# Performance work log

Hardware: AMD Instinct MI355X
Metric: run time of the kernel (lower is better)

Reference implementation:

```python
import jax, jax.numpy as jnp
import numpy as np
from jax import lax

NF = 64
KS = 3
PAD = 1
TOPK = 2
DG = 8          # deformable_groups
N = KS * KS     # 9 sampling points


def conv3x3(x, w, b):
    y = lax.conv_general_dilated(x, w, (1, 1), 'SAME',
                                 dimension_numbers=('NCHW', 'OIHW', 'NCHW'))
    return y + b[None, :, None, None]


def lrelu(x):
    return jnp.where(x >= 0, x, 0.1 * x)


def dsp_sample(x, feat, w_om, b_om):
    """Modulated deformable sampling (DSP_sep2): returns the N bilinearly
    sampled, mask-modulated taps per pixel, shape (B, C, N, H, W)."""
    B, C, H, W = x.shape
    Cg = C // DG
    om = conv3x3(feat, w_om, b_om)              # (B, 3*DG*N, H, W)
    o1, o2, m = jnp.split(om, 3, axis=1)
    off_y = o1.reshape(B, DG, N, H, W)
    off_x = o2.reshape(B, DG, N, H, W)
    mask = jax.nn.sigmoid(m).reshape(B, DG, 1, N, H * W)
    kk = (jnp.arange(KS) - PAD).astype(jnp.float32)
    kdy = jnp.repeat(kk, KS)                    # (N,) kernel row offsets
    kdx = jnp.tile(kk, KS)                      # (N,) kernel col offsets
    ii = jnp.arange(H, dtype=jnp.float32)
    jj = jnp.arange(W, dtype=jnp.float32)
    ys = ii[None, None, None, :, None] + kdy[None, None, :, None, None] + off_y
    xs = jj[None, None, None, None, :] + kdx[None, None, :, None, None] + off_x
    y0 = jnp.floor(ys)
    x0 = jnp.floor(xs)
    xf = x.reshape(B, DG, Cg, H * W)
    out = jnp.zeros((B, DG, Cg, N, H * W), x.dtype)
    # bilinear interpolation with zero padding outside the image
    for dy in (0.0, 1.0):
        for dx in (0.0, 1.0):
            yi = y0 + dy
            xi = x0 + dx
            wgt = (1.0 - jnp.abs(ys - yi)) * (1.0 - jnp.abs(xs - xi))
            valid = (yi >= 0) & (yi <= H - 1) & (xi >= 0) & (xi <= W - 1)
            lin = (jnp.clip(yi, 0, H - 1) * W + jnp.clip(xi, 0, W - 1)).astype(jnp.int32)
            g = jnp.take_along_axis(xf[:, :, :, None, :],
                                    lin.reshape(B, DG, 1, N, H * W), axis=-1)
            out = out + g * jnp.where(valid, wgt, 0.0).reshape(B, DG, 1, N, H * W)
    return (out * mask).reshape(B, C, N, H, W)


def setup_inputs() -> dict:
    key = jax.random.key(0)
    ks = jax.random.split(key, 9)
    B, C, H, W = 2, NF, 192, 192

    def rn(k, s, sc=1.0):
        return jax.random.normal(k, s, jnp.float32) * sc

    return {
        'query': rn(ks[0], (B, C, H, W)),
        'key':   rn(ks[1], (B, C, H, W)),
        'value': rn(ks[2], (B, C, H, W)),
        'w1': rn(ks[3], (C, 2 * C, 3, 3), 0.05), 'b1': rn(ks[4], (C,), 0.05),
        'w2': rn(ks[5], (C, C, 3, 3), 0.05),     'b2': rn(ks[6], (C,), 0.05),
        'w_om': rn(ks[7], (3 * DG * N, C, 3, 3), 0.01),
        'b_om': rn(ks[8], (3 * DG * N,), 0.01),
    }


def reference(query, key, value, w1, b1, w2, b2, w_om, b_om):
    B, C, H, W = query.shape
    HW = H * W
    feat = lrelu(conv3x3(jnp.concatenate([query, key], axis=1), w1, b1))
    feat = lrelu(conv3x3(feat, w2, b2))
    # deformable sampled keys: (B, C, N, H, W) -> (B, HW, N, C)
    key_off = dsp_sample(key, feat, w_om, b_om).transpose(0, 3, 4, 2, 1).reshape(B, HW, N, C)
    q = query.reshape(B, C, HW).transpose(0, 2, 1)            # (B, HW, C)
    rel = jnp.einsum('bpnc,bpc->bpn', key_off, q)             # relevance scores
    topv, topi = lax.top_k(rel, TOPK)                         # (B, HW, TOPK)
    corr = jax.nn.softmax(topv, axis=-1)
    val_off = dsp_sample(value, feat, w_om, b_om).transpose(0, 3, 4, 2, 1).reshape(B, HW, N, C)
    k_sel = jnp.take_along_axis(key_off, topi[..., None], axis=2)  # (B, HW, TOPK, C)
    v_sel = jnp.take_along_axis(val_off, topi[..., None], axis=2)
    k_upd = jnp.einsum('bptc,bpt->bpc', k_sel, corr)
    v_out = jnp.einsum('bptc,bpt->bpc', v_sel, corr).transpose(0, 2, 1)  # (B, C, HW)
    weight = jnp.einsum('bpc,bpc->bp', q, k_upd)              # (B, HW)
    return (weight, v_out)
```

## Files before the change

kernel.cpp:

```cpp
#include <hip/hip_runtime.h>
#include <math.h>

#define H_  192
#define W_  192
#define HW_ (192 * 192)
#define B_  2
#define C_  64
#define PW_ 194

typedef __attribute__((ext_vector_type(8))) short short8;
typedef __attribute__((ext_vector_type(4))) short short4v;
typedef __attribute__((ext_vector_type(4))) float float4v;
typedef _Float16 __attribute__((ext_vector_type(8))) half8;

union hbits { _Float16 f; short s; };
__device__ __forceinline__ void split2(float x, short& h, short& l) {
    _Float16 hf = (_Float16)x;
    float r = (x - (float)hf) * 4096.f;
    _Float16 lf = (_Float16)r;
    hbits u;
    u.f = hf; h = u.s;
    u.f = lf; l = u.s;
}

__device__ __forceinline__ float bilin_dot(const float* __restrict__ pl,
                                           float ys, float xs, int c4,
                                           float4v q4) {
    float y0 = floorf(ys), x0 = floorf(xs);
    float fy = ys - y0, fx = xs - x0;
    int iy = (int)y0, ix = (int)x0;
    float acc = 0.f;
    #pragma unroll
    for (int dy = 0; dy < 2; ++dy) {
        #pragma unroll
        for (int dx = 0; dx < 2; ++dx) {
            int yy = iy + dy, xx = ix + dx;
            float wgt = (dy ? fy : 1.f - fy) * (dx ? fx : 1.f - fx);
            bool valid = (yy >= 0) && (yy < H_) && (xx >= 0) && (xx < W_);
            int yc = min(max(yy, 0), H_ - 1);
            int xc = min(max(xx, 0), W_ - 1);
            const float4v v = *(const float4v*)(pl + (size_t)(yc * W_ + xc) * 64 + c4);
            float d = v[0] * q4[0] + v[1] * q4[1] + v[2] * q4[2] + v[3] * q4[3];
            acc += valid ? wgt * d : 0.f;
        }
    }
    return acc;
}
__device__ __forceinline__ float4v bilin_v4(const float* __restrict__ pl,
                                            float ys, float xs, int c4) {
    float y0 = floorf(ys), x0 = floorf(xs);
    float fy = ys - y0, fx = xs - x0;
    int iy = (int)y0, ix = (int)x0;
    float4v acc;
    acc[0] = acc[1] = acc[2] = acc[3] = 0.f;
    #pragma unroll
    for (int dy = 0; dy < 2; ++dy) {
        #pragma unroll
        for (int dx = 0; dx < 2; ++dx) {
            int yy = iy + dy, xx = ix + dx;
            float wgt = (dy ? fy : 1.f - fy) * (dx ? fx : 1.f - fx);
            bool valid = (yy >= 0) && (yy < H_) && (xx >= 0) && (xx < W_);
            float wz = valid ? wgt : 0.f;
            int yc = min(max(yy, 0), H_ - 1);
            int xc = min(max(xx, 0), W_ - 1);
            const float4v v = *(const float4v*)(pl + (size_t)(yc * W_ + xc) * 64 + c4);
            #pragma unroll
            for (int r = 0; r < 4; ++r) acc[r] += wz * v[r];
        }
    }
    return acc;
}

__global__ __launch_bounds__(256) void prep_w_k(
    const float* __restrict__ w1, const float* __restrict__ w2,
    const float* __restrict__ wom,
    short* __restrict__ pw1, short* __restrict__ pw2, short* __restrict__ pwom)
{
    int idx = blockIdx.x * 256 + threadIdx.x;
    int arr;
    if (idx < 144 * 512) { arr = 0; }
    else if (idx < (144 + 72) * 512) { arr = 1; idx -= 144 * 512; }
    else if (idx < (144 + 72 + 252) * 512) { arr = 2; idx -= (144 + 72) * 512; }
    else return;
    int frag = idx >> 9, within = idx & 511;
    int lane = within >> 3, j = within & 7;
    int KS   = (arr == 0) ? 4 : 2;
    int mt   = frag / (9 * KS);
    int rem  = frag % (9 * KS);
    int kk   = rem / KS;
    int s    = rem % KS;
    int co   = mt * 16 + (lane & 15);
    int c    = s * 32 + (lane >> 4) * 8 + j;
    float v = 0.f;
    if (arr == 0)      v = w1[(co * 128 + c) * 9 + kk];
    else if (arr == 1) v = w2[(co * 64 + c) * 9 + kk];
    else if (co < 216) v = wom[(co * 64 + c) * 9 + kk];
    short h, l;
    split2(v, h, l);
    short* dst = (arr == 0) ? pw1 : (arr == 1) ? pw2 : pwom;
    size_t base = (size_t)frag * 1024 + lane * 8 + j;
    dst[base]       = h;
    dst[base + 512] = l;
}

__global__ __launch_bounds__(256) void pack_qk(
    const float* __restrict__ q, const float* __restrict__ k,
    short* __restrict__ qk2)
{
    __shared__ float sm[128][65];
    const int tid = threadIdx.x;
    const int p0  = blockIdx.x * 64;
    const int b   = blockIdx.y;
    const int pp  = tid & 63;
    const int r0  = tid >> 6;
    #pragma unroll
    for (int c = r0; c < 128; c += 4) {
        const float* src = (c < 64) ? q : k;
        sm[c][pp] = src[(size_t)(b * 64 + (c & 63)) * HW_ + p0 + pp];
    }
    __syncthreads();
    for (int idx = tid; idx < 64 * 128; idx += 256) {
        int pxw = idx >> 7, ci = idx & 127;
        short h, l;
        split2(sm[ci][pxw], h, l);
        int p  = p0 + pxw;
        int rr = p / W_, cc = p - rr * W_;
        short* dstp = qk2 + ((size_t)(b * PW_ + rr + 1) * PW_ + cc + 1) * 256;
        dstp[ci]       = h;
        dstp[128 + ci] = l;
    }
}

__global__ __launch_bounds__(256) void zero_borders(
    short* __restrict__ f1p, short* __restrict__ f2p, short* __restrict__ qk2)
{
    const int prow = blockIdx.x;
    const int b    = blockIdx.y;
    const int z    = blockIdx.z;
    short* dst = (z == 0) ? f1p : (z == 1) ? f2p : qk2;
    const int nc = (z == 2) ? 256 : 128;
    dst += (size_t)(b * PW_ + prow) * PW_ * nc;
    if (prow == 0 || prow == PW_ - 1) {
        for (int idx = threadIdx.x; idx < PW_ * nc; idx += 256) dst[idx] = 0;
    } else {
        for (int idx = threadIdx.x; idx < nc; idx += 256) {
            dst[idx] = 0;
            dst[(size_t)(PW_ - 1) * nc + idx] = 0;
        }
    }
}

__global__ __launch_bounds__(256) void nchw_to_nhwc(
    const float* __restrict__ key, const float* __restrict__ value,
    float* __restrict__ kT, float* __restrict__ vT)
{
    __shared__ float sm[64][65];
    const int tid = threadIdx.x;
    const int p0  = blockIdx.x * 64;
    const int b   = blockIdx.y;
    const float* src = blockIdx.z ? value : key;
    float*       dst = blockIdx.z ? vT    : kT;
    const int pp = tid & 63;
    const int r0 = tid >> 6;
    #pragma unroll
    for (int c = r0; c < 64; c += 4)
        sm[c][pp] = src[(size_t)(b * 64 + c) * HW_ + p0 + pp];
    __syncthreads();
    const int cc = tid & 63;
    #pragma unroll
    for (int pw = r0; pw < 64; pw += 4)
        dst[((size_t)b * HW_ + p0 + pw) * 64 + cc] = sm[cc][pw];
}

template<int CIN, int MT, bool LRELU, int OUTMODE>
__global__ __launch_bounds__(256) void conv_direct(
    const short* __restrict__ in, const short* __restrict__ pw,
    const float* __restrict__ bias, void* __restrict__ outv)
{
    constexpr int KS  = CIN / 32;
    constexpr int MTW = MT / 2;

    const int tid  = threadIdx.x;
    const int lane = tid & 63;
    const int w    = tid >> 6;
    const int wh   = w & 1;
    const int wn   = w >> 1;
    const int quad = lane >> 4;
    const int nn   = lane & 15;

    const int flat = blockIdx.x;
    const int xcd  = flat & 7;
    const int cc_  = flat >> 3;
    const int b    = xcd >> 2;
    const int r4   = xcd & 3;
    const int i    = r4 * 48 + cc_ / 3;
    const int j0   = (cc_ % 3) * 64;
    const int mt0  = wh * MTW;

    constexpr float CSC = 1.f / 4096.f;

    float4v accM[MTW][2];
    #pragma unroll
    for (int m = 0; m < MTW; ++m)
        #pragma unroll
        for (int t = 0; t < 2; ++t)
            #pragma unroll
            for (int r = 0; r < 4; ++r) accM[m][t][r] = 0.f;

    float4v zvec;
    zvec[0] = zvec[1] = zvec[2] = zvec[3] = 0.f;

    for (int ky = 0; ky < 3; ++ky) {
        const short* rowp = in + ((size_t)(b * PW_ + (i + ky)) * PW_) * (2 * CIN);
        #pragma unroll
        for (int kx = 0; kx < 3; ++kx) {
            const int kk = ky * 3 + kx;
            #pragma unroll
            for (int s = 0; s < KS; ++s) {
                half8 bh[2], bl[2];
                #pragma unroll
                for (int t2 = 0; t2 < 2; ++t2) {
                    const int pcol = j0 + kx + (wn * 2 + t2) * 16 + nn;
                    const short* bp = rowp + (size_t)pcol * (2 * CIN)
                                    + s * 32 + quad * 8;
                    bh[t2] = *(const half8*)bp;
                    bl[t2] = *(const half8*)(bp + CIN);
                }
                #pragma unroll
                for (int m = 0; m < MTW; ++m) {
                    const short* ap = pw
                        + ((size_t)(((mt0 + m) * 9 + kk) * KS + s)) * 1024
                        + lane * 8;
                    half8 ah = *(const half8*)ap;
                    half8 al = *(const half8*)(ap + 512);
                    float4v t0, t1;
                    accM[m][0] = __builtin_amdgcn_mfma_f32_16x16x32_f16(ah, bh[0], accM[m][0], 0, 0, 0);
                    t0         = __builtin_amdgcn_mfma_f32_16x16x32_f16(ah, bl[0], zvec,       0, 0, 0);
                    accM[m][1] = __builtin_amdgcn_mfma_f32_16x16x32_f16(ah, bh[1], accM[m][1], 0, 0, 0);
                    t1         = __builtin_amdgcn_mfma_f32_16x16x32_f16(ah, bl[1], zvec,       0, 0, 0);
                    t0         = __builtin_amdgcn_mfma_f32_16x16x32_f16(al, bh[0], t0,         0, 0, 0);
                    t1         = __builtin_amdgcn_mfma_f32_16x16x32_f16(al, bh[1], t1,         0, 0, 0);
                    #pragma unroll
                    for (int r = 0; r < 4; ++r) {
                        accM[m][0][r] += t0[r] * CSC;
                        accM[m][1][r] += t1[r] * CSC;
                    }
                }
            }
        }
    }

    #pragma unroll
    for (int m = 0; m < MTW; ++m) {
        const int co0 = (mt0 + m) * 16 + quad * 4;
        #pragma unroll
        for (int t2 = 0; t2 < 2; ++t2) {
            const int t = wn * 2 + t2;
            if (OUTMODE == 0) {
                const size_t pp = ((size_t)(b * PW_ + i + 1) * PW_
                                   + (j0 + t * 16 + nn + 1)) * 128;
                short* feat = (short*)outv;
                short4v hv, lv;
                #pragma unroll
                for (int r = 0; r < 4; ++r) {
                    float x = accM[m][t2][r] + bias[co0 + r];
                    if (LRELU) x = (x >= 0.f) ? x : 0.1f * x;
                    short h, l;
                    split2(x, h, l);
                    hv[r] = h; lv[r] = l;
                }
                *(short4v*)(feat + pp + co0)      = hv;
                *(short4v*)(feat + pp + 64 + co0) = lv;
            } else {
                if (co0 < 216) {
                    const int p = i * W_ + j0 + t * 16 + nn;
                    float* om = (float*)outv;
                    float4v v;
                    #pragma unroll
                    for (int r = 0; r < 4; ++r)
                        v[r] = accM[m][t2][r] + bias[co0 + r];
                    *(float4v*)(om + ((size_t)b * HW_ + p) * 216 + co0) = v;
                }
            }
        }
    }
}

__global__ __launch_bounds__(256) void sampler_k(
    const float* __restrict__ query, const float* __restrict__ kT,
    const float* __restrict__ vT, const float* __restrict__ om,
    float* __restrict__ out_w, float* __restrict__ out_v)
{
    __shared__ float sq[16 * 68];
    const int tid  = threadIdx.x;
    const int bb   = blockIdx.x;
    const int b    = bb / 2304;
    const int pblk = (bb - b * 2304) * 16;

    #pragma unroll
    for (int k = 0; k < 4; ++k) {
        int idx = tid + k * 256;
        int c   = idx >> 4;
        int px  = idx & 15;
        sq[px * 68 + c] = query[(size_t)(b * 64 + c) * HW_ + pblk + px];
    }
    __syncthreads();

    const int lane   = tid & 63;
    const int w      = tid >> 6;
    const int px_sub = lane >> 4;
    const int cl     = lane & 15;
    const int c4     = cl * 4;
    const int g      = cl >> 1;
    const int p      = pblk + w * 4 + px_sub;
    const int i      = p / W_;
    const int j      = p - i * W_;

    const float4v q4 = *(const float4v*)&sq[(w * 4 + px_sub) * 68 + c4];

    const float* omb = om + ((size_t)b * HW_ + p) * 216;
    float offy[9], offx[9], mk[9];
    #pragma unroll
    for (int n = 0; n < 9; ++n) {
        offy[n] = omb[g * 9 + n];
        offx[n] = omb[72 + g * 9 + n];
        float mv = omb[144 + g * 9 + n];
        mk[n] = 1.f / (1.f + expf(-mv));
    }

    const float* kpl = kT + (size_t)b * HW_ * 64;
    float rel[9];
    #pragma unroll
    for (int n = 0; n < 9; ++n) {
        float ys = (float)i + (float)(n / 3 - 1) + offy[n];
        float xs = (float)j + (float)(n % 3 - 1) + offx[n];
        float d = bilin_dot(kpl, ys, xs, c4, q4) * mk[n];
        #pragma unroll
        for (int off = 1; off < 16; off <<= 1)
            d += __shfl_xor(d, off, 64);
        rel[n] = d;
    }

    int n0 = 0; float v0 = rel[0];
    #pragma unroll
    for (int n = 1; n < 9; ++n) { if (rel[n] > v0) { v0 = rel[n]; n0 = n; } }
    int n1 = -1; float v1 = -1e30f;
    #pragma unroll
    for (int n = 0; n < 9; ++n) { if (n != n0 && rel[n] > v1) { v1 = rel[n]; n1 = n; } }

    float e1  = expf(v1 - v0);
    float inv = 1.f / (1.f + e1);
    float c0 = inv, c1 = e1 * inv;

    if (cl == 0) out_w[(size_t)b * HW_ + p] = c0 * v0 + c1 * v1;

    float oy0 = 0, ox0 = 0, m0 = 0, oy1 = 0, ox1 = 0, m1 = 0;
    #pragma unroll
    for (int n = 0; n < 9; ++n) {
        if (n == n0) { oy0 = offy[n]; ox0 = offx[n]; m0 = mk[n]; }
        if (n == n1) { oy1 = offy[n]; ox1 = offx[n]; m1 = mk[n]; }
    }

    const float* vpl = vT + (size_t)b * HW_ * 64;
    float ys0 = (float)i + (float)(n0 / 3 - 1) + oy0;
    float xs0 = (float)j + (float)(n0 % 3 - 1) + ox0;
    float ys1 = (float)i + (float)(n1 / 3 - 1) + oy1;
    float xs1 = (float)j + (float)(n1 % 3 - 1) + ox1;
    float4v vv0 = bilin_v4(vpl, ys0, xs0, c4);
    float4v vv1 = bilin_v4(vpl, ys1, xs1, c4);
    float w0 = c0 * m0, w1s = c1 * m1;
    #pragma unroll
    for (int r = 0; r < 4; ++r)
        out_v[(size_t)(b * C_ + c4 + r) * HW_ + p] = w0 * vv0[r] + w1s * vv1[r];
}

extern "C" void kernel_launch(void* const* d_in, const int* in_sizes, int n_in,
                              void* d_out, int out_size, void* d_ws, size_t ws_size,
                              hipStream_t stream)
{
    const float* query = (const float*)d_in[0];
    const float* key   = (const float*)d_in[1];
    const float* value = (const float*)d_in[2];
    const float* w1    = (const float*)d_in[3];
    const float* b1    = (const float*)d_in[4];
    const float* w2    = (const float*)d_in[5];
    const float* b2    = (const float*)d_in[6];
    const float* wom   = (const float*)d_in[7];
    const float* bom   = (const float*)d_in[8];
    float* out = (float*)d_out;

    char* ws = (char*)d_ws;
    float* om   = (float*)(ws);
    short* f1p  = (short*)(ws);
    short* qk2  = (short*)(ws + 19269632);
    short* pw1  = (short*)(ws + 57808896);
    short* pw2  = (short*)(ws + 58103808);
    short* f2p  = (short*)(ws + 63700992);
    short* pwom = (short*)(ws + 82970624);
    float* kT   = (float*)(ws + 63700992);
    float* vT   = (float*)(ws + 82575360);

    zero_borders<<<dim3(PW_, B_, 3), 256, 0, stream>>>(f1p, f2p, qk2);
    pack_qk<<<dim3(HW_ / 64, B_), 256, 0, stream>>>(query, key, qk2);
    prep_w_k<<<936, 256, 0, stream>>>(w1, w2, wom, pw1, pw2, pwom);

    conv_direct<128, 4,  true,  0><<<1152, 256, 0, stream>>>(qk2, pw1, b1, (void*)f1p);
    conv_direct<64,  4,  true,  0><<<1152, 256, 0, stream>>>(f1p, pw2, b2, (void*)f2p);
    conv_direct<64,  14, false, 1><<<1152, 256, 0, stream>>>(f2p, pwom, bom, (void*)om);

    nchw_to_nhwc<<<dim3(576, B_, 2), 256, 0, stream>>>(key, value, kT, vT);

    float* out_w = out;
    float* out_v = out + (size_t)B_ * HW_;
    sampler_k<<<(B_ * HW_) / 16, 256, 0, stream>>>(query, kT, vT, om, out_w, out_v);
}
```

Before: 468.5 us.

## Software-pipeline B-fragment loads in conv MFMA loop and XCD-map pack_qk blocks

The conv_direct inner loop is flattened over (ky,kx,s) and fully unrolled, with the activation fragments for the next iteration loaded ahead while the current MFMAs run. This is meant to hide global-load latency behind the matrix math, at the cost of extra registers for the double-buffered fragments. pack_qk now uses the same XCD-aware block-to-tile mapping as the conv kernels, so the qk2 tiles each die writes are the ones its conv blocks later read from that die's L2, and the per-pixel divide is removed.

```diff
diff --git a/kernel.cpp b/kernel.cpp
--- a/kernel.cpp
+++ b/kernel.cpp
@@ -108,11 +108,17 @@
     short* __restrict__ qk2)
 {
     __shared__ float sm[128][65];
-    const int tid = threadIdx.x;
-    const int p0  = blockIdx.x * 64;
-    const int b   = blockIdx.y;
-    const int pp  = tid & 63;
-    const int r0  = tid >> 6;
+    const int tid  = threadIdx.x;
+    const int flat = blockIdx.x;
+    const int xcd  = flat & 7;
+    const int cc_  = flat >> 3;
+    const int b    = xcd >> 2;
+    const int r4   = xcd & 3;
+    const int i    = r4 * 48 + cc_ / 3;
+    const int j0   = (cc_ % 3) * 64;
+    const int p0   = i * W_ + j0;
+    const int pp   = tid & 63;
+    const int r0   = tid >> 6;
     #pragma unroll
     for (int c = r0; c < 128; c += 4) {
         const float* src = (c < 64) ? q : k;
@@ -123,9 +129,7 @@
         int pxw = idx >> 7, ci = idx & 127;
         short h, l;
         split2(sm[ci][pxw], h, l);
-        int p  = p0 + pxw;
-        int rr = p / W_, cc = p - rr * W_;
-        short* dstp = qk2 + ((size_t)(b * PW_ + rr + 1) * PW_ + cc + 1) * 256;
+        short* dstp = qk2 + ((size_t)(b * PW_ + i + 1) * PW_ + j0 + pxw + 1) * 256;
         dstp[ci]       = h;
         dstp[128 + ci] = l;
     }
@@ -179,6 +183,7 @@
 {
     constexpr int KS  = CIN / 32;
     constexpr int MTW = MT / 2;
+    constexpr int NT  = 9 * KS;
 
     const int tid  = threadIdx.x;
     const int lane = tid & 63;
@@ -210,44 +215,68 @@
     float4v zvec;
     zvec[0] = zvec[1] = zvec[2] = zvec[3] = 0.f;
 
-    for (int ky = 0; ky < 3; ++ky) {
-        const short* rowp = in + ((size_t)(b * PW_ + (i + ky)) * PW_) * (2 * CIN);
-        #pragma unroll
-        for (int kx = 0; kx < 3; ++kx) {
-            const int kk = ky * 3 + kx;
+    auto baddr = [&](int it, int t2) -> const short* {
+        const int ky = it / (3 * KS);
+        const int rm = it % (3 * KS);
+        const int kx = rm / KS;
+        const int s  = rm % KS;
+        const int pcol = j0 + kx + (wn * 2 + t2) * 16 + nn;
+        return in + ((size_t)(b * PW_ + i + ky) * PW_ + pcol) * (2 * CIN)
+                  + s * 32 + quad * 8;
+    };
+
+    half8 bhc[2], blc[2];
+    #pragma unroll
+    for (int t2 = 0; t2 < 2; ++t2) {
+        const short* bp = baddr(0, t2);
+        bhc[t2] = *(const half8*)bp;
+        blc[t2] = *(const half8*)(bp + CIN);
+    }
+
+    #pragma unroll
+    for (int it = 0; it < NT; ++it) {
+        half8 bhn[2], bln[2];
+        if (it + 1 < NT) {
             #pragma unroll
-            for (int s = 0; s < KS; ++s) {
-                half8 bh[2], bl[2];
-                #pragma unroll
-                for (int t2 = 0; t2 < 2; ++t2) {
-                    const int pcol = j0 + kx + (wn * 2 + t2) * 16 + nn;
-                    const short* bp = rowp + (size_t)pcol * (2 * CIN)
-                                    + s * 32 + quad * 8;
-                    bh[t2] = *(const half8*)bp;
-                    bl[t2] = *(const half8*)(bp + CIN);
-                }
-                #pragma unroll
-                for (int m = 0; m < MTW; ++m) {
-                    const short* ap = pw
-                        + ((size_t)(((mt0 + m) * 9 + kk) * KS + s)) * 1024
-                        + lane * 8;
-                    half8 ah = *(const half8*)ap;
-                    half8 al = *(const half8*)(ap + 512);
-                    float4v t0, t1;
-                    accM[m][0] = __builtin_amdgcn_mfma_f32_16x16x32_f16(ah, bh[0], accM[m][0], 0, 0, 0);
-                    t0         = __builtin_amdgcn_mfma_f32_16x16x32_f16(ah, bl[0], zvec,       0, 0, 0);
-                    accM[m][1] = __builtin_amdgcn_mfma_f32_16x16x32_f16(ah, bh[1], accM[m][1], 0, 0, 0);
-                    t1         = __builtin_amdgcn_mfma_f32_16x16x32_f16(ah, bl[1], zvec,       0, 0, 0);
-                    t0         = __builtin_amdgcn_mfma_f32_16x16x32_f16(al, bh[0], t0,         0, 0, 0);
-                    t1         = __builtin_amdgcn_mfma_f32_16x16x32_f16(al, bh[1], t1,         0, 0, 0);
-                    #pragma unroll
-                    for (int r = 0; r < 4; ++r) {
-                        accM[m][0][r] += t0[r] * CSC;
-                        accM[m][1][r] += t1[r] * CSC;
-                    }
-                }
+            for (int t2 = 0; t2 < 2; ++t2) {
+                const short* bp = baddr(it + 1, t2);
+                bhn[t2] = *(const half8*)bp;
+                bln[t2] = *(const half8*)(bp + CIN);
             }
-        }
+        } else {
+            #pragma unroll
+            for (int t2 = 0; t2 < 2; ++t2) { bhn[t2] = bhc[t2]; bln[t2] = blc[t2]; }
+        }
+
+        const int ky = it / (3 * KS);
+        const int rm = it % (3 * KS);
+        const int kx = rm / KS;
+        const int s  = rm % KS;
+        const int kk = ky * 3 + kx;
+
+        #pragma unroll
+        for (int m = 0; m < MTW; ++m) {
+            const short* ap = pw
+                + ((size_t)(((mt0 + m) * 9 + kk) * KS + s)) * 1024
+                + lane * 8;
+            half8 ah = *(const half8*)ap;
+            half8 al = *(const half8*)(ap + 512);
+            float4v t0, t1;
+            accM[m][0] = __builtin_amdgcn_mfma_f32_16x16x32_f16(ah, bhc[0], accM[m][0], 0, 0, 0);
+            t0         = __builtin_amdgcn_mfma_f32_16x16x32_f16(ah, blc[0], zvec,       0, 0, 0);
+            accM[m][1] = __builtin_amdgcn_mfma_f32_16x16x32_f16(ah, bhc[1], accM[m][1], 0, 0, 0);
+            t1         = __builtin_amdgcn_mfma_f32_16x16x32_f16(ah, blc[1], zvec,       0, 0, 0);
+            t0         = __builtin_amdgcn_mfma_f32_16x16x32_f16(al, bhc[0], t0,         0, 0, 0);
+            t1         = __builtin_amdgcn_mfma_f32_16x16x32_f16(al, bhc[1], t1,         0, 0, 0);
+            #pragma unroll
+            for (int r = 0; r < 4; ++r) {
+                accM[m][0][r] += t0[r] * CSC;
+                accM[m][1][r] += t1[r] * CSC;
+            }
+        }
+
+        #pragma unroll
+        for (int t2 = 0; t2 < 2; ++t2) { bhc[t2] = bhn[t2]; blc[t2] = bln[t2]; }
     }
 
     #pragma unroll
@@ -401,7 +430,7 @@
     float* vT   = (float*)(ws + 82575360);
 
     zero_borders<<<dim3(PW_, B_, 3), 256, 0, stream>>>(f1p, f2p, qk2);
-    pack_qk<<<dim3(HW_ / 64, B_), 256, 0, stream>>>(query, key, qk2);
+    pack_qk<<<1152, 256, 0, stream>>>(query, key, qk2);
     prep_w_k<<<936, 256, 0, stream>>>(w1, w2, wom, pw1, pw2, pwom);
 
     conv_direct<128, 4,  true,  0><<<1152, 256, 0, stream>>>(qk2, pw1, b1, (void*)f1p);
```

Result: no change. 462.2 us (-1.3%).
